# Kernel tuning notes

Hardware: AMD Instinct MI355X
Metric: run time of the kernel (lower is better)

Reference implementation:

```python
import jax, jax.numpy as jnp
import numpy as np
import math

CH = 256
HEADS = 4
GROUPS = 8
EPS = 1e-5


def group_norm(x, gamma, beta):
    # x: [B, C, H, W], normalize over (C//G, H, W) per group
    B, C, H, W = x.shape
    xg = x.reshape(B, GROUPS, C // GROUPS, H, W)
    mean = xg.mean(axis=(2, 3, 4), keepdims=True)
    var = xg.var(axis=(2, 3, 4), keepdims=True)
    xn = ((xg - mean) * jax.lax.rsqrt(var + EPS)).reshape(B, C, H, W)
    return xn * gamma[None, :, None, None] + beta[None, :, None, None]


def setup_inputs() -> dict:
    key = jax.random.key(0)
    ks = jax.random.split(key, 7)
    B, C, H, W = 4, CH, 64, 64
    x = jax.random.normal(ks[0], (B, C, H, W), dtype=jnp.float32)
    norm_w = jnp.ones((C,), dtype=jnp.float32)
    norm_b = jnp.zeros((C,), dtype=jnp.float32)
    s = 1.0 / math.sqrt(C)
    qkv_w = jax.random.normal(ks[1], (3 * C, C), dtype=jnp.float32) * s  # 1x1 conv kernel
    qkv_b = jnp.zeros((3 * C,), dtype=jnp.float32)
    proj_w = jax.random.normal(ks[2], (C, C), dtype=jnp.float32) * s
    proj_b = jnp.zeros((C,), dtype=jnp.float32)
    return {"x": x, "norm_w": norm_w, "norm_b": norm_b,
            "qkv_w": qkv_w, "qkv_b": qkv_b,
            "proj_w": proj_w, "proj_b": proj_b}


def reference(x, norm_w, norm_b, qkv_w, qkv_b, proj_w, proj_b):
    B, C, H, W = x.shape
    d = C // HEADS
    h = group_norm(x, norm_w, norm_b)
    # 1x1 conv == channel matmul
    qkv = jnp.einsum('oc,bchw->bohw', qkv_w, h) + qkv_b[None, :, None, None]
    qkv = qkv.reshape(B, 3, HEADS, d, H * W)
    q, k, v = qkv[:, 0], qkv[:, 1], qkv[:, 2]  # [B, heads, d, HW]
    attn = jnp.einsum('bhdi,bhdj->bhij', q, k) / jnp.sqrt(jnp.float32(d))
    attn = jax.nn.softmax(attn, axis=-1)
    out = jnp.einsum('bhij,bhdj->bhdi', attn, v).reshape(B, C, H, W)
    out = jnp.einsum('oc,bchw->bohw', proj_w, out) + proj_b[None, :, None, None]
    return x + out
```

## Files before the change

### kernel.cpp

```cpp
#include <hip/hip_runtime.h>
#include <stdint.h>

#define NB    4
#define CC    256
#define NN    4096
#define NHEAD 4
#define DH    64
#define NGRP  8
#define GSIZE 131072

typedef unsigned short u16;
typedef __attribute__((ext_vector_type(8))) short s16x8;
typedef __attribute__((ext_vector_type(4))) float f32x4;

__device__ __forceinline__ u16 f2b(float f) {
  uint32_t x = __float_as_uint(f);
  x += 0x7fffu + ((x >> 16) & 1u);
  return (u16)(x >> 16);
}

__device__ __forceinline__ uint32_t pk2(float a, float b) {
  uint32_t r;
  asm("v_cvt_pk_bf16_f32 %0, %1, %2" : "=v"(r) : "v"(a), "v"(b));
  return r;
}

__global__ __launch_bounds__(256) void k_prep(const float* __restrict__ qw,
                                              const float* __restrict__ pw,
                                              u16* __restrict__ qwb,
                                              u16* __restrict__ pwb,
                                              float* __restrict__ stats) {
  int i = blockIdx.x * 256 + threadIdx.x;
  if (i < 64) stats[i] = 0.f;
  for (int idx = i; idx < 3 * CC * CC; idx += 65536) qwb[idx] = f2b(qw[idx]);
  if (i < CC * CC) pwb[i] = f2b(pw[i]);
}

__global__ __launch_bounds__(256) void k_gn_stats(const float* __restrict__ x,
                                                  float* __restrict__ stats) {
  int grp = blockIdx.x >> 4, sub = blockIdx.x & 15;
  const float4* p4 = (const float4*)(x + (size_t)grp * GSIZE + (size_t)sub * 8192);
  float s = 0.f, s2 = 0.f;
#pragma unroll
  for (int i = 0; i < 8; ++i) {
    float4 v = p4[threadIdx.x + 256 * i];
    s  += v.x + v.y + v.z + v.w;
    s2 += v.x * v.x + v.y * v.y + v.z * v.z + v.w * v.w;
  }
#pragma unroll
  for (int off = 1; off < 64; off <<= 1) { s += __shfl_xor(s, off); s2 += __shfl_xor(s2, off); }
  __shared__ float red[8];
  int w = threadIdx.x >> 6;
  if ((threadIdx.x & 63) == 0) { red[w] = s; red[4 + w] = s2; }
  __syncthreads();
  if (threadIdx.x == 0) {
    s  = red[0] + red[1] + red[2] + red[3];
    s2 = red[4] + red[5] + red[6] + red[7];
    atomicAdd(&stats[grp], s);
    atomicAdd(&stats[32 + grp], s2);
  }
}

__global__ __launch_bounds__(256) void k_gn_norm(const float* __restrict__ x,
                                                 const float* __restrict__ stats,
                                                 const float* __restrict__ gw,
                                                 const float* __restrict__ gb,
                                                 u16* __restrict__ ht) {
  __shared__ u16 T[64 * 72];
  int b = blockIdx.z, cb = blockIdx.y, nb = blockIdx.x;
  int t = threadIdx.x;
  int c = t >> 2, nch = (t & 3) * 16;
  int cg = cb * 64 + c;
  int grp = b * NGRP + (cg >> 5);
  float mean = stats[grp] * (1.f / (float)GSIZE);
  float var  = stats[32 + grp] * (1.f / (float)GSIZE) - mean * mean;
  float rstd = rsqrtf(var + 1e-5f);
  float ga = gw[cg] * rstd;
  float be = gb[cg] - mean * ga;
  const float* px = x + ((size_t)b * CC + cg) * NN + nb * 64 + nch;
#pragma unroll
  for (int k = 0; k < 4; ++k) {
    float4 v = *(const float4*)(px + 4 * k);
    int nl = nch + 4 * k;
    T[(nl + 0) * 72 + c] = f2b(v.x * ga + be);
    T[(nl + 1) * 72 + c] = f2b(v.y * ga + be);
    T[(nl + 2) * 72 + c] = f2b(v.z * ga + be);
    T[(nl + 3) * 72 + c] = f2b(v.w * ga + be);
  }
  __syncthreads();
  int n = t >> 2, cch = (t & 3) * 16;
  u16* dst = ht + ((size_t)b * NN + nb * 64 + n) * CC + cb * 64 + cch;
  *(uint4*)(dst)     = *(const uint4*)&T[n * 72 + cch];
  *(uint4*)(dst + 8) = *(const uint4*)&T[n * 72 + cch + 8];
}

__global__ __launch_bounds__(256) void k_qkv(const u16* __restrict__ Aw,
                                             const float* __restrict__ bias,
                                             const u16* __restrict__ ht,
                                             u16* __restrict__ Qt,
                                             u16* __restrict__ Kt,
                                             u16* __restrict__ Vv) {
  __shared__ u16 sm[5120];
  u16* As = sm;
  u16* Bs = sm + 2560;
  int b = blockIdx.z, bm = blockIdx.y, bn = blockIdx.x;
  int t = threadIdx.x, w = t >> 6, lane = t & 63, lr = lane & 15, lg = lane >> 4;
  int wm = w >> 1, wn = w & 1;
  int srow = t >> 2, sch = (t & 3) * 8;
  const u16* Ap = Aw + (size_t)(bm * 64 + srow) * CC + sch;
  const u16* Bp = ht + ((size_t)b * NN + bn * 64 + srow) * CC + sch;
  f32x4 acc[2][2] = {};
  for (int kt = 0; kt < CC / 32; ++kt) {
    *(uint4*)&As[srow * 40 + sch] = *(const uint4*)(Ap + kt * 32);
    *(uint4*)&Bs[srow * 40 + sch] = *(const uint4*)(Bp + kt * 32);
    __syncthreads();
    s16x8 af[2], bf[2];
#pragma unroll
    for (int fm = 0; fm < 2; ++fm) af[fm] = *(const s16x8*)&As[(wm * 32 + fm * 16 + lr) * 40 + lg * 8];
#pragma unroll
    for (int fn = 0; fn < 2; ++fn) bf[fn] = *(const s16x8*)&Bs[(wn * 32 + fn * 16 + lr) * 40 + lg * 8];
#pragma unroll
    for (int fm = 0; fm < 2; ++fm)
#pragma unroll
      for (int fn = 0; fn < 2; ++fn)
        acc[fm][fn] = __builtin_amdgcn_mfma_f32_16x16x32_bf16(af[fm], bf[fn], acc[fm][fn], 0, 0, 0);
    __syncthreads();
  }
  int which = bm >> 2, head = bm & 3;
  if (which == 2) {
#pragma unroll
    for (int fm = 0; fm < 2; ++fm)
#pragma unroll
      for (int fn = 0; fn < 2; ++fn)
#pragma unroll
        for (int r = 0; r < 4; ++r) {
          int m = wm * 32 + fm * 16 + lg * 4 + r;
          int n = wn * 32 + fn * 16 + lr;
          float v = acc[fm][fn][r] + bias[bm * 64 + m];
          Vv[((size_t)(b * NHEAD + head) * DH + m) * NN + bn * 64 + n] = f2b(v);
        }
  } else {
    u16* Ts = sm;
    float scale = (which == 0) ? 0.125f * 1.44269504f : 1.0f;
#pragma unroll
    for (int fm = 0; fm < 2; ++fm)
#pragma unroll
      for (int fn = 0; fn < 2; ++fn)
#pragma unroll
        for (int r = 0; r < 4; ++r) {
          int m = wm * 32 + fm * 16 + lg * 4 + r;
          int n = wn * 32 + fn * 16 + lr;
          float v = (acc[fm][fn][r] + bias[bm * 64 + m]) * scale;
          Ts[n * 72 + m] = f2b(v);
        }
    __syncthreads();
    u16* dst = (which == 0 ? Qt : Kt);
    int n = t >> 2, cch = (t & 3) * 16;
    u16* o = dst + ((size_t)(b * NHEAD + head) * NN + bn * 64 + n) * DH + cch;
    *(uint4*)(o)     = *(const uint4*)&Ts[n * 72 + cch];
    *(uint4*)(o + 8) = *(const uint4*)&Ts[n * 72 + cch + 8];
  }
}

__global__ __launch_bounds__(256, 4) void k_attn(const u16* __restrict__ Qt,
                                                 const u16* __restrict__ Kt,
                                                 const u16* __restrict__ Vv,
                                                 u16* __restrict__ att) {
  __shared__ __align__(16) u16 Ks[128 * 72];
  __shared__ __align__(16) u16 Vs[64 * 136];
  int bh = blockIdx.y, qt = blockIdx.x;
  int t = threadIdx.x, w = t >> 6, lane = t & 63, lr = lane & 15, lg = lane >> 4;
  const u16* Qb = Qt + ((size_t)bh * NN + qt * 64 + w * 16) * DH;
  const u16* Kb = Kt + (size_t)bh * NN * DH;
  const u16* Vb = Vv + (size_t)bh * DH * NN;
  s16x8 bq[2];
#pragma unroll
  for (int kk = 0; kk < 2; ++kk) bq[kk] = *(const s16x8*)(Qb + lr * DH + kk * 32 + lg * 8);
  const s16x8 ones = (s16x8)(short)0x3F80;
  float m = -1e30f;
  f32x4 oacc[4] = {};
  f32x4 lacc = {};
  int srK = t >> 1, scK = (t & 1) * 32;
  int wK = srK & 63;
  int prK = (srK & 64) | (wK & 32) | (((wK >> 2) & 3) << 3) | (((wK >> 4) & 1) << 2) | (wK & 3);
  const u16* kp0 = Kb + (size_t)prK * DH + scK;
  u16* ksw = &Ks[srK * 72 + scK];
  int srV = t >> 2, scV = (t & 3) * 32;
  const u16* vp0 = Vb + (size_t)srV * NN + scV;
  u16* vsw = &Vs[srV * 136 + scV];
  {
    uint4 a0 = *(const uint4*)(kp0),      a1 = *(const uint4*)(kp0 + 8);
    uint4 a2 = *(const uint4*)(kp0 + 16), a3 = *(const uint4*)(kp0 + 24);
    uint4 b0 = *(const uint4*)(vp0),      b1 = *(const uint4*)(vp0 + 8);
    uint4 b2 = *(const uint4*)(vp0 + 16), b3 = *(const uint4*)(vp0 + 24);
    *(uint4*)(ksw) = a0; *(uint4*)(ksw + 8) = a1; *(uint4*)(ksw + 16) = a2; *(uint4*)(ksw + 24) = a3;
    *(uint4*)(vsw) = b0; *(uint4*)(vsw + 8) = b1; *(uint4*)(vsw + 16) = b2; *(uint4*)(vsw + 24) = b3;
  }
  __syncthreads();
  for (int j0 = 0; j0 < NN; j0 += 128) {
    int jn = (j0 + 128 < NN) ? j0 + 128 : 0;
    const u16* kp = kp0 + (size_t)jn * DH;
    const u16* vp = vp0 + jn;
    uint4 rka = *(const uint4*)(kp),      rkb = *(const uint4*)(kp + 8);
    uint4 rkc = *(const uint4*)(kp + 16), rkd = *(const uint4*)(kp + 24);
    uint4 rva = *(const uint4*)(vp),      rvb = *(const uint4*)(vp + 8);
    uint4 rvc = *(const uint4*)(vp + 16), rvd = *(const uint4*)(vp + 24);
    f32x4 s[8];
    __builtin_amdgcn_s_setprio(1);
#pragma unroll
    for (int q = 0; q < 8; ++q) {
      const u16* base = &Ks[(q * 16 + lr) * 72 + lg * 8];
      s16x8 a0 = *(const s16x8*)(base);
      s16x8 a1 = *(const s16x8*)(base + 32);
      f32x4 z = {};
      z = __builtin_amdgcn_mfma_f32_16x16x32_bf16(a0, bq[0], z, 0, 0, 0);
      z = __builtin_amdgcn_mfma_f32_16x16x32_bf16(a1, bq[1], z, 0, 0, 0);
      s[q] = z;
    }
    __builtin_amdgcn_s_setprio(0);
    float mx = fmaxf(s[0][0], s[0][1]);
    mx = fmaxf(mx, fmaxf(s[0][2], s[0][3]));
#pragma unroll
    for (int q = 1; q < 8; ++q) {
      mx = fmaxf(mx, fmaxf(s[q][0], s[q][1]));
      mx = fmaxf(mx, fmaxf(s[q][2], s[q][3]));
    }
    mx = fmaxf(mx, __shfl_xor(mx, 16));
    mx = fmaxf(mx, __shfl_xor(mx, 32));
    if (__any(mx > m + 8.f)) {
      float mnew  = fmaxf(m, mx);
      float alpha = exp2f(m - mnew);
#pragma unroll
      for (int dt = 0; dt < 4; ++dt)
#pragma unroll
        for (int r = 0; r < 4; ++r) oacc[dt][r] *= alpha;
#pragma unroll
      for (int r = 0; r < 4; ++r) lacc[r] *= alpha;
      m = mnew;
    }
    union { s16x8 v; uint32_t u[4]; } pb[4];
#pragma unroll
    for (int q = 0; q < 8; ++q) {
      float p0 = exp2f(s[q][0] - m);
      float p1 = exp2f(s[q][1] - m);
      float p2 = exp2f(s[q][2] - m);
      float p3 = exp2f(s[q][3] - m);
      int c = (q >> 2) * 2 + ((q >> 1) & 1);
      pb[c].u[(q & 1) * 2]     = pk2(p0, p1);
      pb[c].u[(q & 1) * 2 + 1] = pk2(p2, p3);
    }
    __builtin_amdgcn_s_setprio(1);
#pragma unroll
    for (int dt = 0; dt < 4; ++dt) {
      const u16* vb2 = &Vs[(dt * 16 + lr) * 136 + lg * 8];
#pragma unroll
      for (int c = 0; c < 4; ++c) {
        s16x8 av = *(const s16x8*)(vb2 + c * 32);
        oacc[dt] = __builtin_amdgcn_mfma_f32_16x16x32_bf16(av, pb[c].v, oacc[dt], 0, 0, 0);
      }
    }
#pragma unroll
    for (int c = 0; c < 4; ++c)
      lacc = __builtin_amdgcn_mfma_f32_16x16x32_bf16(ones, pb[c].v, lacc, 0, 0, 0);
    __builtin_amdgcn_s_setprio(0);
    __syncthreads();
    *(uint4*)(ksw) = rka; *(uint4*)(ksw + 8) = rkb; *(uint4*)(ksw + 16) = rkc; *(uint4*)(ksw + 24) = rkd;
    *(uint4*)(vsw) = rva; *(uint4*)(vsw + 8) = rvb; *(uint4*)(vsw + 16) = rvc; *(uint4*)(vsw + 24) = rvd;
    __syncthreads();
  }
  float linv = 1.f / lacc[0];
  int b = bh >> 2, h = bh & 3;
  u16* ob = att + ((size_t)b * NN + qt * 64 + w * 16 + lr) * CC + h * 64 + lg * 4;
#pragma unroll
  for (int dt = 0; dt < 4; ++dt) {
    uint2 pkd;
    pkd.x = pk2(oacc[dt][0] * linv, oacc[dt][1] * linv);
    pkd.y = pk2(oacc[dt][2] * linv, oacc[dt][3] * linv);
    *(uint2*)(ob + dt * 16) = pkd;
  }
}

__global__ __launch_bounds__(256) void k_proj(const u16* __restrict__ Aw,
                                              const float* __restrict__ bias,
                                              const u16* __restrict__ att,
                                              const float* __restrict__ x,
                                              float* __restrict__ out) {
  __shared__ u16 sm[5120];
  u16* As = sm;
  u16* Bs = sm + 2560;
  int b = blockIdx.z, bm = blockIdx.y, bn = blockIdx.x;
  int t = threadIdx.x, w = t >> 6, lane = t & 63, lr = lane & 15, lg = lane >> 4;
  int wm = w >> 1, wn = w & 1;
  int srow = t >> 2, sch = (t & 3) * 8;
  const u16* Ap = Aw + (size_t)(bm * 64 + srow) * CC + sch;
  const u16* Bp = att + ((size_t)b * NN + bn * 64 + srow) * CC + sch;
  f32x4 acc[2][2] = {};
  for (int kt = 0; kt < CC / 32; ++kt) {
    *(uint4*)&As[srow * 40 + sch] = *(const uint4*)(Ap + kt * 32);
    *(uint4*)&Bs[srow * 40 + sch] = *(const uint4*)(Bp + kt * 32);
    __syncthreads();
    s16x8 af[2], bf[2];
#pragma unroll
    for (int fm = 0; fm < 2; ++fm) af[fm] = *(const s16x8*)&As[(wm * 32 + fm * 16 + lr) * 40 + lg * 8];
#pragma unroll
    for (int fn = 0; fn < 2; ++fn) bf[fn] = *(const s16x8*)&Bs[(wn * 32 + fn * 16 + lr) * 40 + lg * 8];
#pragma unroll
    for (int fm = 0; fm < 2; ++fm)
#pragma unroll
      for (int fn = 0; fn < 2; ++fn)
        acc[fm][fn] = __builtin_amdgcn_mfma_f32_16x16x32_bf16(af[fm], bf[fn], acc[fm][fn], 0, 0, 0);
    __syncthreads();
  }
#pragma unroll
  for (int fm = 0; fm < 2; ++fm)
#pragma unroll
    for (int fn = 0; fn < 2; ++fn)
#pragma unroll
      for (int r = 0; r < 4; ++r) {
        int o = bm * 64 + wm * 32 + fm * 16 + lg * 4 + r;
        int n = bn * 64 + wn * 32 + fn * 16 + lr;
        size_t idx = ((size_t)b * CC + o) * NN + n;
        out[idx] = x[idx] + bias[o] + acc[fm][fn][r];
      }
}

extern "C" void kernel_launch(void* const* d_in, const int* in_sizes, int n_in,
                              void* d_out, int out_size, void* d_ws, size_t ws_size,
                              hipStream_t stream) {
  const float* x  = (const float*)d_in[0];
  const float* nw = (const float*)d_in[1];
  const float* nb = (const float*)d_in[2];
  const float* qw = (const float*)d_in[3];
  const float* qb = (const float*)d_in[4];
  const float* pw = (const float*)d_in[5];
  const float* pb = (const float*)d_in[6];
  float* out = (float*)d_out;
  char* ws = (char*)d_ws;
  float* stats = (float*)(ws + 0);
  u16* qwb = (u16*)(ws + 4096);
  u16* pwb = (u16*)(ws + 397312);
  u16* ht  = (u16*)(ws + 528384);
  u16* Qt  = (u16*)(ws + 8916992);
  u16* Kt  = (u16*)(ws + 17305600);
  u16* Vv  = (u16*)(ws + 25694208);
  u16* att = (u16*)(ws + 34082816);

  k_prep<<<dim3(256), dim3(256), 0, stream>>>(qw, pw, qwb, pwb, stats);
  k_gn_stats<<<dim3(512), dim3(256), 0, stream>>>(x, stats);
  k_gn_norm<<<dim3(64, 4, NB), dim3(256), 0, stream>>>(x, stats, nw, nb, ht);
  k_qkv<<<dim3(64, 12, NB), dim3(256), 0, stream>>>(qwb, qb, ht, Qt, Kt, Vv);
  k_attn<<<dim3(64, NB * NHEAD), dim3(256), 0, stream>>>(Qt, Kt, Vv, att);
  k_proj<<<dim3(64, 4, NB), dim3(256), 0, stream>>>(pwb, pb, att, x, out);
}
```

Baseline: 175.8 us.

## Process two 16-row query tiles per wave in attention to reuse K/V LDS loads

Each wave in the attention kernel now handles 32 query rows (two 16-row tiles) instead of 16, so a block covers 128 queries and the grid halves to 32 blocks per head. Every K and V fragment read from shared memory now feeds two MFMAs, which halves the LDS traffic and the global K/V streaming per query. The cost is double the accumulator and score registers, so launch bounds drop to 2 blocks per SM. With only 512 blocks, occupancy and latency hiding may suffer.

```diff
diff --git a/kernel.cpp b/kernel.cpp
--- a/kernel.cpp
+++ b/kernel.cpp
@@ -162,7 +162,7 @@
   }
 }
 
-__global__ __launch_bounds__(256, 4) void k_attn(const u16* __restrict__ Qt,
+__global__ __launch_bounds__(256, 2) void k_attn(const u16* __restrict__ Qt,
                                                  const u16* __restrict__ Kt,
                                                  const u16* __restrict__ Vv,
                                                  u16* __restrict__ att) {
@@ -170,16 +170,19 @@
   __shared__ __align__(16) u16 Vs[64 * 136];
   int bh = blockIdx.y, qt = blockIdx.x;
   int t = threadIdx.x, w = t >> 6, lane = t & 63, lr = lane & 15, lg = lane >> 4;
-  const u16* Qb = Qt + ((size_t)bh * NN + qt * 64 + w * 16) * DH;
+  const u16* Qb = Qt + ((size_t)bh * NN + qt * 128 + w * 32) * DH;
   const u16* Kb = Kt + (size_t)bh * NN * DH;
   const u16* Vb = Vv + (size_t)bh * DH * NN;
-  s16x8 bq[2];
-#pragma unroll
-  for (int kk = 0; kk < 2; ++kk) bq[kk] = *(const s16x8*)(Qb + lr * DH + kk * 32 + lg * 8);
+  s16x8 bq0[2], bq1[2];
+#pragma unroll
+  for (int kk = 0; kk < 2; ++kk) {
+    bq0[kk] = *(const s16x8*)(Qb + lr * DH + kk * 32 + lg * 8);
+    bq1[kk] = *(const s16x8*)(Qb + (16 + lr) * DH + kk * 32 + lg * 8);
+  }
   const s16x8 ones = (s16x8)(short)0x3F80;
-  float m = -1e30f;
-  f32x4 oacc[4] = {};
-  f32x4 lacc = {};
+  float m0 = -1e30f, m1 = -1e30f;
+  f32x4 oacc[2][4] = {};
+  f32x4 la0 = {}, la1 = {};
   int srK = t >> 1, scK = (t & 1) * 32;
   int wK = srK & 63;
   int prK = (srK & 64) | (wK & 32) | (((wK >> 2) & 3) << 3) | (((wK >> 4) & 1) << 2) | (wK & 3);
@@ -205,49 +208,85 @@
     uint4 rkc = *(const uint4*)(kp + 16), rkd = *(const uint4*)(kp + 24);
     uint4 rva = *(const uint4*)(vp),      rvb = *(const uint4*)(vp + 8);
     uint4 rvc = *(const uint4*)(vp + 16), rvd = *(const uint4*)(vp + 24);
-    f32x4 s[8];
+    f32x4 s0[8], s1[8];
     __builtin_amdgcn_s_setprio(1);
 #pragma unroll
     for (int q = 0; q < 8; ++q) {
       const u16* base = &Ks[(q * 16 + lr) * 72 + lg * 8];
       s16x8 a0 = *(const s16x8*)(base);
       s16x8 a1 = *(const s16x8*)(base + 32);
-      f32x4 z = {};
-      z = __builtin_amdgcn_mfma_f32_16x16x32_bf16(a0, bq[0], z, 0, 0, 0);
-      z = __builtin_amdgcn_mfma_f32_16x16x32_bf16(a1, bq[1], z, 0, 0, 0);
-      s[q] = z;
+      f32x4 z0 = {}, z1 = {};
+      z0 = __builtin_amdgcn_mfma_f32_16x16x32_bf16(a0, bq0[0], z0, 0, 0, 0);
+      z1 = __builtin_amdgcn_mfma_f32_16x16x32_bf16(a0, bq1[0], z1, 0, 0, 0);
+      z0 = __builtin_amdgcn_mfma_f32_16x16x32_bf16(a1, bq0[1], z0, 0, 0, 0);
+      z1 = __builtin_amdgcn_mfma_f32_16x16x32_bf16(a1, bq1[1], z1, 0, 0, 0);
+      s0[q] = z0; s1[q] = z1;
     }
     __builtin_amdgcn_s_setprio(0);
-    float mx = fmaxf(s[0][0], s[0][1]);
-    mx = fmaxf(mx, fmaxf(s[0][2], s[0][3]));
-#pragma unroll
-    for (int q = 1; q < 8; ++q) {
-      mx = fmaxf(mx, fmaxf(s[q][0], s[q][1]));
-      mx = fmaxf(mx, fmaxf(s[q][2], s[q][3]));
-    }
-    mx = fmaxf(mx, __shfl_xor(mx, 16));
-    mx = fmaxf(mx, __shfl_xor(mx, 32));
-    if (__any(mx > m + 8.f)) {
-      float mnew  = fmaxf(m, mx);
-      float alpha = exp2f(m - mnew);
-#pragma unroll
-      for (int dt = 0; dt < 4; ++dt)
-#pragma unroll
-        for (int r = 0; r < 4; ++r) oacc[dt][r] *= alpha;
-#pragma unroll
-      for (int r = 0; r < 4; ++r) lacc[r] *= alpha;
-      m = mnew;
-    }
-    union { s16x8 v; uint32_t u[4]; } pb[4];
-#pragma unroll
-    for (int q = 0; q < 8; ++q) {
-      float p0 = exp2f(s[q][0] - m);
-      float p1 = exp2f(s[q][1] - m);
-      float p2 = exp2f(s[q][2] - m);
-      float p3 = exp2f(s[q][3] - m);
-      int c = (q >> 2) * 2 + ((q >> 1) & 1);
-      pb[c].u[(q & 1) * 2]     = pk2(p0, p1);
-      pb[c].u[(q & 1) * 2 + 1] = pk2(p2, p3);
+    union { s16x8 v; uint32_t u[4]; } pb0[4], pb1[4];
+    {
+      float mx = fmaxf(s0[0][0], s0[0][1]);
+      mx = fmaxf(mx, fmaxf(s0[0][2], s0[0][3]));
+#pragma unroll
+      for (int q = 1; q < 8; ++q) {
+        mx = fmaxf(mx, fmaxf(s0[q][0], s0[q][1]));
+        mx = fmaxf(mx, fmaxf(s0[q][2], s0[q][3]));
+      }
+      mx = fmaxf(mx, __shfl_xor(mx, 16));
+      mx = fmaxf(mx, __shfl_xor(mx, 32));
+      if (__any(mx > m0 + 8.f)) {
+        float mnew  = fmaxf(m0, mx);
+        float alpha = exp2f(m0 - mnew);
+#pragma unroll
+        for (int dt = 0; dt < 4; ++dt)
+#pragma unroll
+          for (int r = 0; r < 4; ++r) oacc[0][dt][r] *= alpha;
+#pragma unroll
+        for (int r = 0; r < 4; ++r) la0[r] *= alpha;
+        m0 = mnew;
+      }
+#pragma unroll
+      for (int q = 0; q < 8; ++q) {
+        float p0 = exp2f(s0[q][0] - m0);
+        float p1 = exp2f(s0[q][1] - m0);
+        float p2 = exp2f(s0[q][2] - m0);
+        float p3 = exp2f(s0[q][3] - m0);
+        int c = (q >> 2) * 2 + ((q >> 1) & 1);
+        pb0[c].u[(q & 1) * 2]     = pk2(p0, p1);
+        pb0[c].u[(q & 1) * 2 + 1] = pk2(p2, p3);
+      }
+    }
+    {
+      float mx = fmaxf(s1[0][0], s1[0][1]);
+      mx = fmaxf(mx, fmaxf(s1[0][2], s1[0][3]));
+#pragma unroll
+      for (int q = 1; q < 8; ++q) {
+        mx = fmaxf(mx, fmaxf(s1[q][0], s1[q][1]));
+        mx = fmaxf(mx, fmaxf(s1[q][2], s1[q][3]));
+      }
+      mx = fmaxf(mx, __shfl_xor(mx, 16));
+      mx = fmaxf(mx, __shfl_xor(mx, 32));
+      if (__any(mx > m1 + 8.f)) {
+        float mnew  = fmaxf(m1, mx);
+        float alpha = exp2f(m1 - mnew);
+#pragma unroll
+        for (int dt = 0; dt < 4; ++dt)
+#pragma unroll
+          for (int r = 0; r < 4; ++r) oacc[1][dt][r] *= alpha;
+#pragma unroll
+        for (int r = 0; r < 4; ++r) la1[r] *= alpha;
+        m1 = mnew;
+      }
+#pragma unroll
+      for (int q = 0; q < 8; ++q) {
+        float p0 = exp2f(s1[q][0] - m1);
+        float p1 = exp2f(s1[q][1] - m1);
+        float p2 = exp2f(s1[q][2] - m1);
+        float p3 = exp2f(s1[q][3] - m1);
+        int c = (q >> 2) * 2 + ((q >> 1) & 1);
+        pb1[c].u[(q & 1) * 2]     = pk2(p0, p1);
+        pb1[c].u[(q & 1) * 2 + 1] = pk2(p2, p3);
+      }
     }
     __builtin_amdgcn_s_setprio(1);
 #pragma unroll
@@ -256,27 +295,34 @@
 #pragma unroll
       for (int c = 0; c < 4; ++c) {
         s16x8 av = *(const s16x8*)(vb2 + c * 32);
-        oacc[dt] = __builtin_amdgcn_mfma_f32_16x16x32_bf16(av, pb[c].v, oacc[dt], 0, 0, 0);
-      }
-    }
-#pragma unroll
-    for (int c = 0; c < 4; ++c)
-      lacc = __builtin_amdgcn_mfma_f32_16x16x32_bf16(ones, pb[c].v, lacc, 0, 0, 0);
+        oacc[0][dt] = __builtin_amdgcn_mfma_f32_16x16x32_bf16(av, pb0[c].v, oacc[0][dt], 0, 0, 0);
+        oacc[1][dt] = __builtin_amdgcn_mfma_f32_16x16x32_bf16(av, pb1[c].v, oacc[1][dt], 0, 0, 0);
+      }
+    }
+#pragma unroll
+    for (int c = 0; c < 4; ++c) {
+      la0 = __builtin_amdgcn_mfma_f32_16x16x32_bf16(ones, pb0[c].v, la0, 0, 0, 0);
+      la1 = __builtin_amdgcn_mfma_f32_16x16x32_bf16(ones, pb1[c].v, la1, 0, 0, 0);
+    }
     __builtin_amdgcn_s_setprio(0);
     __syncthreads();
     *(uint4*)(ksw) = rka; *(uint4*)(ksw + 8) = rkb; *(uint4*)(ksw + 16) = rkc; *(uint4*)(ksw + 24) = rkd;
     *(uint4*)(vsw) = rva; *(uint4*)(vsw + 8) = rvb; *(uint4*)(vsw + 16) = rvc; *(uint4*)(vsw + 24) = rvd;
     __syncthreads();
   }
-  float linv = 1.f / lacc[0];
   int b = bh >> 2, h = bh & 3;
-  u16* ob = att + ((size_t)b * NN + qt * 64 + w * 16 + lr) * CC + h * 64 + lg * 4;
-#pragma unroll
-  for (int dt = 0; dt < 4; ++dt) {
-    uint2 pkd;
-    pkd.x = pk2(oacc[dt][0] * linv, oacc[dt][1] * linv);
-    pkd.y = pk2(oacc[dt][2] * linv, oacc[dt][3] * linv);
-    *(uint2*)(ob + dt * 16) = pkd;
+#pragma unroll
+  for (int g = 0; g < 2; ++g) {
+    float linv = 1.f / (g ? la1[0] : la0[0]);
+    u16* ob = att + ((size_t)b * NN + qt * 128 + w * 32 + g * 16 + lr) * CC + h * 64 + lg * 4;
+#pragma unroll
+    for (int dt = 0; dt < 4; ++dt) {
+      f32x4 oa = oacc[g][dt];
+      uint2 pkd;
+      pkd.x = pk2(oa[0] * linv, oa[1] * linv);
+      pkd.y = pk2(oa[2] * linv, oa[3] * linv);
+      *(uint2*)(ob + dt * 16) = pkd;
+    }
   }
 }
 
@@ -349,6 +395,6 @@
   k_gn_stats<<<dim3(512), dim3(256), 0, stream>>>(x, stats);
   k_gn_norm<<<dim3(64, 4, NB), dim3(256), 0, stream>>>(x, stats, nw, nb, ht);
   k_qkv<<<dim3(64, 12, NB), dim3(256), 0, stream>>>(qwb, qb, ht, Qt, Kt, Vv);
-  k_attn<<<dim3(64, NB * NHEAD), dim3(256), 0, stream>>>(Qt, Kt, Vv, att);
+  k_attn<<<dim3(32, NB * NHEAD), dim3(256), 0, stream>>>(Qt, Kt, Vv, att);
   k_proj<<<dim3(64, 4, NB), dim3(256), 0, stream>>>(pwb, pb, att, x, out);
 }
```

Result: no change. 177.4 us (+0.9%).

## Load V fragments directly from global memory and remap attention blocks per XCD

Applied to the files above, without the earlier changes.

The attention kernel stops staging V through shared memory. Each wave now reads its V MFMA operands straight from global memory into registers, with the next d-tile prefetched while the current one is multiplied. The grid is flattened to 1D and remapped so that blocks of the same batch-head land on the same XCD, which should improve L2 reuse of K and V. This cuts LDS traffic and footprint, but each wave now issues redundant global loads of V, and those loads are exposed to latency inside the inner loop.

```diff
diff --git a/kernel.cpp b/kernel.cpp
--- a/kernel.cpp
+++ b/kernel.cpp
@@ -167,8 +167,10 @@
                                                  const u16* __restrict__ Vv,
                                                  u16* __restrict__ att) {
   __shared__ __align__(16) u16 Ks[128 * 72];
-  __shared__ __align__(16) u16 Vs[64 * 136];
-  int bh = blockIdx.y, qt = blockIdx.x;
+  int lin = blockIdx.x;
+  int xcd = lin & 7, idx = lin >> 3;
+  int bh = xcd * 2 + (idx >> 6);
+  int qt = idx & 63;
   int t = threadIdx.x, w = t >> 6, lane = t & 63, lr = lane & 15, lg = lane >> 4;
   const u16* Qb = Qt + ((size_t)bh * NN + qt * 64 + w * 16) * DH;
   const u16* Kb = Kt + (size_t)bh * NN * DH;
@@ -185,26 +187,18 @@
   int prK = (srK & 64) | (wK & 32) | (((wK >> 2) & 3) << 3) | (((wK >> 4) & 1) << 2) | (wK & 3);
   const u16* kp0 = Kb + (size_t)prK * DH + scK;
   u16* ksw = &Ks[srK * 72 + scK];
-  int srV = t >> 2, scV = (t & 3) * 32;
-  const u16* vp0 = Vb + (size_t)srV * NN + scV;
-  u16* vsw = &Vs[srV * 136 + scV];
+  const u16* vr0 = Vb + (size_t)lr * NN + lg * 8;
   {
     uint4 a0 = *(const uint4*)(kp0),      a1 = *(const uint4*)(kp0 + 8);
     uint4 a2 = *(const uint4*)(kp0 + 16), a3 = *(const uint4*)(kp0 + 24);
-    uint4 b0 = *(const uint4*)(vp0),      b1 = *(const uint4*)(vp0 + 8);
-    uint4 b2 = *(const uint4*)(vp0 + 16), b3 = *(const uint4*)(vp0 + 24);
     *(uint4*)(ksw) = a0; *(uint4*)(ksw + 8) = a1; *(uint4*)(ksw + 16) = a2; *(uint4*)(ksw + 24) = a3;
-    *(uint4*)(vsw) = b0; *(uint4*)(vsw + 8) = b1; *(uint4*)(vsw + 16) = b2; *(uint4*)(vsw + 24) = b3;
   }
   __syncthreads();
   for (int j0 = 0; j0 < NN; j0 += 128) {
     int jn = (j0 + 128 < NN) ? j0 + 128 : 0;
     const u16* kp = kp0 + (size_t)jn * DH;
-    const u16* vp = vp0 + jn;
     uint4 rka = *(const uint4*)(kp),      rkb = *(const uint4*)(kp + 8);
     uint4 rkc = *(const uint4*)(kp + 16), rkd = *(const uint4*)(kp + 24);
-    uint4 rva = *(const uint4*)(vp),      rvb = *(const uint4*)(vp + 8);
-    uint4 rvc = *(const uint4*)(vp + 16), rvd = *(const uint4*)(vp + 24);
     f32x4 s[8];
     __builtin_amdgcn_s_setprio(1);
 #pragma unroll
@@ -218,6 +212,10 @@
       s[q] = z;
     }
     __builtin_amdgcn_s_setprio(0);
+    const u16* vj = vr0 + j0;
+    s16x8 va[4], vn[4];
+#pragma unroll
+    for (int c = 0; c < 4; ++c) va[c] = *(const s16x8*)(vj + c * 32);
     float mx = fmaxf(s[0][0], s[0][1]);
     mx = fmaxf(mx, fmaxf(s[0][2], s[0][3]));
 #pragma unroll
@@ -252,12 +250,16 @@
     __builtin_amdgcn_s_setprio(1);
 #pragma unroll
     for (int dt = 0; dt < 4; ++dt) {
-      const u16* vb2 = &Vs[(dt * 16 + lr) * 136 + lg * 8];
-#pragma unroll
-      for (int c = 0; c < 4; ++c) {
-        s16x8 av = *(const s16x8*)(vb2 + c * 32);
-        oacc[dt] = __builtin_amdgcn_mfma_f32_16x16x32_bf16(av, pb[c].v, oacc[dt], 0, 0, 0);
+      if (dt < 3) {
+        const u16* vnx = vj + (size_t)(dt + 1) * 16 * NN;
+#pragma unroll
+        for (int c = 0; c < 4; ++c) vn[c] = *(const s16x8*)(vnx + c * 32);
       }
+#pragma unroll
+      for (int c = 0; c < 4; ++c)
+        oacc[dt] = __builtin_amdgcn_mfma_f32_16x16x32_bf16(va[c], pb[c].v, oacc[dt], 0, 0, 0);
+#pragma unroll
+      for (int c = 0; c < 4; ++c) va[c] = vn[c];
     }
 #pragma unroll
     for (int c = 0; c < 4; ++c)
@@ -265,7 +267,6 @@
     __builtin_amdgcn_s_setprio(0);
     __syncthreads();
     *(uint4*)(ksw) = rka; *(uint4*)(ksw + 8) = rkb; *(uint4*)(ksw + 16) = rkc; *(uint4*)(ksw + 24) = rkd;
-    *(uint4*)(vsw) = rva; *(uint4*)(vsw + 8) = rvb; *(uint4*)(vsw + 16) = rvc; *(uint4*)(vsw + 24) = rvd;
     __syncthreads();
   }
   float linv = 1.f / lacc[0];
@@ -349,6 +350,6 @@
   k_gn_stats<<<dim3(512), dim3(256), 0, stream>>>(x, stats);
   k_gn_norm<<<dim3(64, 4, NB), dim3(256), 0, stream>>>(x, stats, nw, nb, ht);
   k_qkv<<<dim3(64, 12, NB), dim3(256), 0, stream>>>(qwb, qb, ht, Qt, Kt, Vv);
-  k_attn<<<dim3(64, NB * NHEAD), dim3(256), 0, stream>>>(Qt, Kt, Vv, att);
+  k_attn<<<dim3(1024), dim3(256), 0, stream>>>(Qt, Kt, Vv, att);
   k_proj<<<dim3(64, 4, NB), dim3(256), 0, stream>>>(pwb, pb, att, x, out);
 }
```

New measurement: 315.2 us. 79.3% more time.
